# Optimization experiments

Hardware: AMD Instinct MI355X
Metric: run time of the kernel (lower is better)

Reference implementation:

```python
import jax, jax.numpy as jnp
import numpy as np

NUM_HEADS = 16
HEAD_DIM = 64
Q_DIM = K_DIM = V_DIM = 1024
LQ = LK = 4096
TAU = HEAD_DIM ** (-0.5)


def setup_inputs() -> dict:
    key = jax.random.key(0)
    ks = jax.random.split(key, 11)
    inner = NUM_HEADS * HEAD_DIM
    s = 0.02
    return {
        "q": jax.random.normal(ks[0], (LQ, Q_DIM), dtype=jnp.float32),
        "k": jax.random.normal(ks[1], (LK, K_DIM), dtype=jnp.float32),
        "v": jax.random.normal(ks[2], (LK, V_DIM), dtype=jnp.float32),
        "Wq": jax.random.normal(ks[3], (Q_DIM, inner), dtype=jnp.float32) * s,
        "bq": jax.random.normal(ks[4], (inner,), dtype=jnp.float32) * s,
        "Wk": jax.random.normal(ks[5], (K_DIM, inner), dtype=jnp.float32) * s,
        "bk": jax.random.normal(ks[6], (inner,), dtype=jnp.float32) * s,
        "Wv": jax.random.normal(ks[7], (V_DIM, inner), dtype=jnp.float32) * s,
        "bv": jax.random.normal(ks[8], (inner,), dtype=jnp.float32) * s,
        "Wo": jax.random.normal(ks[9], (inner, Q_DIM), dtype=jnp.float32) * s,
        "bo": jax.random.normal(ks[10], (Q_DIM,), dtype=jnp.float32) * s,
    }


def reference(q, k, v, Wq, bq, Wk, bk, Wv, bv, Wo, bo):
    h, x = NUM_HEADS, HEAD_DIM
    # projections: [L, h*x] -> per-head layout
    qh = (q @ Wq + bq).reshape(-1, h, x)  # [Lq, h, x]
    kh = (k @ Wk + bk).reshape(-1, h, x)  # [Lk, h, x]
    vh = (v @ Wv + bv).reshape(-1, h, x)  # [Lk, h, x]
    # scores: [h, Lq, Lk]
    att = jnp.einsum('qhx,khx->hqk', qh, kh) * TAU
    att = jax.nn.softmax(att, axis=-1)  # dropout=0.0 -> identity
    ctx = jnp.einsum('hqk,khx->qhx', att, vh).reshape(-1, h * x)  # [Lq, h*x]
    out = ctx @ Wo + bo  # [Lq, Q_DIM]
    return out, att
```

## Files before the change

### kernel.cpp

```cpp
#include <hip/hip_runtime.h>
#include <hip/hip_bf16.h>

typedef unsigned short ushort_t;
typedef __attribute__((ext_vector_type(8))) short short8;
typedef __attribute__((ext_vector_type(8))) __bf16 bf16x8;
typedef __attribute__((ext_vector_type(4))) float f32x4;

#define LQS 4096
#define LKS 4096
#define NH 16
#define HD 64
#define DIN 1024
#define QBLK 64
#define KVB 64
static constexpr float TAU_S = 0.125f;
static constexpr float LOG2E = 1.4426950408889634f;

__device__ __forceinline__ float exp2_fast(float x) { return __builtin_amdgcn_exp2f(x); }

__device__ __forceinline__ ushort_t f32_to_bf16(float x) {
  union { float f; unsigned u; } v; v.f = x;
  unsigned r = v.u + 0x7FFF + ((v.u >> 16) & 1);
  return (ushort_t)(r >> 16);
}

__device__ __forceinline__ void gld_lds16(const void* g, void* l) {
  __builtin_amdgcn_global_load_lds((const __attribute__((address_space(1))) void*)g,
                                   (__attribute__((address_space(3))) void*)l, 16, 0, 0);
}

__device__ __forceinline__ f32x4 mfma16(bf16x8 a, bf16x8 b, f32x4 c) {
  return __builtin_amdgcn_mfma_f32_16x16x32_bf16(a, b, c, 0, 0, 0);
}

struct Cvt3 { const float* src[3]; ushort_t* dst[3]; };
__global__ void cvt_kernel(Cvt3 c) {
  const float* __restrict__ src = c.src[blockIdx.y];
  ushort_t* __restrict__ dst = c.dst[blockIdx.y];
  int i = (blockIdx.x * 256 + threadIdx.x) * 8;
  float4 a = *(const float4*)(src + i);
  float4 b = *(const float4*)(src + i + 4);
  short8 o;
  o[0] = (short)f32_to_bf16(a.x); o[1] = (short)f32_to_bf16(a.y);
  o[2] = (short)f32_to_bf16(a.z); o[3] = (short)f32_to_bf16(a.w);
  o[4] = (short)f32_to_bf16(b.x); o[5] = (short)f32_to_bf16(b.y);
  o[6] = (short)f32_to_bf16(b.z); o[7] = (short)f32_to_bf16(b.w);
  *(short8*)(dst + i) = o;
}

struct TW4 { const float* W[4]; ushort_t* Wt[4]; };
__global__ void transpose_w(TW4 w) {
  const float* __restrict__ W = w.W[blockIdx.z];
  ushort_t* __restrict__ Wt = w.Wt[blockIdx.z];
  __shared__ float tile[64][65];
  const int t = threadIdx.x;
  const int k0 = blockIdx.y * 64, n0 = blockIdx.x * 64;
#pragma unroll
  for (int i = 0; i < 16; ++i) {
    int idx = i * 256 + t;
    int r = idx >> 6, c = idx & 63;
    tile[r][c] = W[(size_t)(k0 + r) * DIN + n0 + c];
  }
  __syncthreads();
#pragma unroll
  for (int i = 0; i < 16; ++i) {
    int idx = i * 256 + t;
    int r = idx >> 6, c = idx & 63;
    Wt[(size_t)(n0 + r) * DIN + k0 + c] = f32_to_bf16(tile[c][r]);
  }
}

__global__ void transpose_v(const ushort_t* __restrict__ vh, ushort_t* __restrict__ vt) {
  __shared__ ushort_t tile[64][65];
  const int t = threadIdx.x;
  const int k0 = blockIdx.x * 64, h = blockIdx.y;
#pragma unroll
  for (int i = 0; i < 16; ++i) {
    int idx = i * 256 + t;
    int r = idx >> 6, c = idx & 63;
    tile[r][c] = vh[(size_t)(k0 + r) * DIN + h * HD + c];
  }
  __syncthreads();
#pragma unroll
  for (int i = 0; i < 16; ++i) {
    int idx = i * 256 + t;
    int r = idx >> 6, c = idx & 63;
    vt[((size_t)h * HD + r) * (size_t)LKS + k0 + c] = tile[c][r];
  }
}

struct Batch3 {
  const ushort_t* A[3];
  const ushort_t* Bt[3];
  const float* bias[3];
  void* C[3];
  float scale[3];
};
template <bool OUT_F32>
__launch_bounds__(256, 2)
__global__ void gemm_nt(Batch3 bt3) {
  const int bid = blockIdx.x;
  const int xcd = bid & 7, idx = bid >> 3;
  const int z = idx >> 5, rem = idx & 31;
  const int by = xcd * 4 + (rem >> 3), bx = rem & 7;
  const ushort_t* __restrict__ A = bt3.A[z];
  const ushort_t* __restrict__ Bt = bt3.Bt[z];
  const float* __restrict__ bias = bt3.bias[z];
  void* __restrict__ Cout = bt3.C[z];
  const float scale = bt3.scale[z];
  const int K = DIN, N = DIN;

  __shared__ __align__(16) ushort_t Alds[128 * 64];
  __shared__ __align__(16) ushort_t Blds[128 * 64];
  const int t = threadIdx.x, wave = t >> 6, lane = t & 63;
  const int l15 = lane & 15, lg = lane >> 4;
  const int m0 = by * 128, n0 = bx * 128;
  const int wr = wave >> 1, wc = wave & 1;
  f32x4 acc[4][4];
#pragma unroll
  for (int i = 0; i < 4; ++i)
#pragma unroll
    for (int j = 0; j < 4; ++j) acc[i][j] = (f32x4){0.f, 0.f, 0.f, 0.f};

  for (int tk = 0; tk < K / 64; ++tk) {
#pragma unroll
    for (int c = 0; c < 4; ++c) {
      int chunk = wave * 4 + c;
      int row = chunk * 8 + (lane >> 3);
      int ss = (lane & 7) ^ (row & 7);
      gld_lds16(A + (size_t)(m0 + row) * K + tk * 64 + ss * 8, (char*)Alds + chunk * 1024);
      gld_lds16(Bt + (size_t)(n0 + row) * K + tk * 64 + ss * 8, (char*)Blds + chunk * 1024);
    }
    __syncthreads();
#pragma unroll
    for (int kk = 0; kk < 2; ++kk) {
      bf16x8 a[4], b[4];
#pragma unroll
      for (int i = 0; i < 4; ++i) {
        int ra = wr * 64 + i * 16 + l15;
        a[i] = *(const bf16x8*)((const char*)Alds + ra * 128 + ((((kk * 4 + lg) << 4)) ^ ((ra & 7) << 4)));
        int rb = wc * 64 + i * 16 + l15;
        b[i] = *(const bf16x8*)((const char*)Blds + rb * 128 + ((((kk * 4 + lg) << 4)) ^ ((rb & 7) << 4)));
      }
#pragma unroll
      for (int mi = 0; mi < 4; ++mi)
#pragma unroll
        for (int ni = 0; ni < 4; ++ni)
          acc[mi][ni] = mfma16(a[mi], b[ni], acc[mi][ni]);
    }
    __syncthreads();
  }
#pragma unroll
  for (int ni = 0; ni < 4; ++ni) {
    int coln = n0 + wc * 64 + ni * 16 + l15;
    float bv = bias[coln];
#pragma unroll
    for (int mi = 0; mi < 4; ++mi) {
#pragma unroll
      for (int r = 0; r < 4; ++r) {
        int rowm = m0 + wr * 64 + mi * 16 + lg * 4 + r;
        float v = (acc[mi][ni][r] + bv) * scale;
        if (OUT_F32)
          ((float*)Cout)[(size_t)rowm * N + coln] = v;
        else
          ((ushort_t*)Cout)[(size_t)rowm * N + coln] = f32_to_bf16(v);
      }
    }
  }
}

__launch_bounds__(256, 4)
__global__ void attn_kernel(const ushort_t* __restrict__ qh, const ushort_t* __restrict__ kh,
                            const ushort_t* __restrict__ vt, float* __restrict__ att,
                            ushort_t* __restrict__ ctx) {
  __shared__ __align__(16) ushort_t Klds[KVB * 64];
  __shared__ __align__(16) ushort_t Vlds[KVB * 64];
  __shared__ __align__(16) float Patt[4][16 * 64];
  const int t = threadIdx.x, wave = t >> 6, lane = t & 63;
  const int l15 = lane & 15, lg = lane >> 4;
  const int bid = blockIdx.x;
  const int xcd = bid & 7, idx = bid >> 3;
  const int h = xcd * 2 + (idx >> 6);
  const int q0 = (idx & 63) * QBLK;

  char* Pw = (char*)Patt[wave];

  bf16x8 qa[2];
  {
    int row = q0 + wave * 16 + l15;
    const ushort_t* qp = qh + (size_t)row * DIN + h * HD + lg * 8;
    qa[0] = *(const bf16x8*)(qp);
    qa[1] = *(const bf16x8*)(qp + 32);
  }

  const int srow8 = lane >> 3;
  const int sslot = (lane & 7);

  float rs[4] = {0.f, 0.f, 0.f, 0.f};
  for (int tk = 0; tk < LKS / KVB; ++tk) {
#pragma unroll
    for (int c = 0; c < 2; ++c) {
      int chunk = wave * 2 + c;
      int row = chunk * 8 + srow8;
      int ss = sslot ^ (row & 7);
      gld_lds16(kh + (size_t)(tk * KVB + row) * DIN + h * HD + ss * 8, (char*)Klds + chunk * 1024);
    }
    __syncthreads();
#pragma unroll
    for (int ct = 0; ct < 4; ++ct) {
      f32x4 acc = (f32x4){0.f, 0.f, 0.f, 0.f};
#pragma unroll
      for (int kk = 0; kk < 2; ++kk) {
        int row = ct * 16 + l15;
        bf16x8 kb = *(const bf16x8*)((const char*)Klds + row * 128 + ((((kk * 4 + lg) << 4)) ^ ((row & 7) << 4)));
        acc = mfma16(qa[kk], kb, acc);
      }
#pragma unroll
      for (int r = 0; r < 4; ++r) rs[r] += exp2_fast(acc[r]);
    }
    __syncthreads();
  }
#pragma unroll
  for (int m = 1; m < 16; m <<= 1) {
#pragma unroll
    for (int r = 0; r < 4; ++r) rs[r] += __shfl_xor(rs[r], m, 64);
  }
  float recip[4];
#pragma unroll
  for (int r = 0; r < 4; ++r) recip[r] = 1.0f / rs[r];

  f32x4 cacc[4];
#pragma unroll
  for (int x = 0; x < 4; ++x) cacc[x] = (f32x4){0.f, 0.f, 0.f, 0.f};
  float* atth = att + ((size_t)h << 24);

  for (int tk = 0; tk < LKS / KVB; ++tk) {
#pragma unroll
    for (int c = 0; c < 2; ++c) {
      int chunk = wave * 2 + c;
      int row = chunk * 8 + srow8;
      int ss = sslot ^ (row & 7);
      gld_lds16(kh + (size_t)(tk * KVB + row) * DIN + h * HD + ss * 8, (char*)Klds + chunk * 1024);
      gld_lds16(vt + ((size_t)h * HD + row) * (size_t)LKS + tk * KVB + ss * 8, (char*)Vlds + chunk * 1024);
    }
    __syncthreads();
#pragma unroll
    for (int ct = 0; ct < 4; ++ct) {
      f32x4 acc = (f32x4){0.f, 0.f, 0.f, 0.f};
#pragma unroll
      for (int kk = 0; kk < 2; ++kk) {
        int row = ct * 16 + l15;
        bf16x8 kb = *(const bf16x8*)((const char*)Klds + row * 128 + ((((kk * 4 + lg) << 4)) ^ ((row & 7) << 4)));
        acc = mfma16(qa[kk], kb, acc);
      }
#pragma unroll
      for (int r = 0; r < 4; ++r) {
        float p = exp2_fast(acc[r]) * recip[r];
        int R = lg * 4 + r;
        int col = ct * 16 + l15;
        int slot = col >> 2;
        *(float*)(Pw + R * 256 + (((slot ^ R)) << 4) + (col & 3) * 4) = p;
      }
    }
#pragma unroll
    for (int i = 0; i < 4; ++i) {
      int slot = lg + 4 * i;
      f32x4 v = *(const f32x4*)(Pw + l15 * 256 + ((slot ^ l15) << 4));
      int rowq = q0 + wave * 16 + l15;
      *(f32x4*)(atth + (((size_t)rowq) << 12) + tk * KVB + slot * 4) = v;
    }
    bf16x8 pa[2];
#pragma unroll
    for (int kk = 0; kk < 2; ++kk) {
      int s0 = kk * 8 + lg * 2;
      f32x4 lo = *(const f32x4*)(Pw + l15 * 256 + ((s0 ^ l15) << 4));
      f32x4 hi = *(const f32x4*)(Pw + l15 * 256 + (((s0 + 1) ^ l15) << 4));
      short8 sp;
#pragma unroll
      for (int j = 0; j < 4; ++j) {
        sp[j] = (short)f32_to_bf16(lo[j]);
        sp[4 + j] = (short)f32_to_bf16(hi[j]);
      }
      pa[kk] = *(bf16x8*)&sp;
    }
#pragma unroll
    for (int x = 0; x < 4; ++x) {
#pragma unroll
      for (int kk = 0; kk < 2; ++kk) {
        int rv = x * 16 + l15;
        bf16x8 vb = *(const bf16x8*)((const char*)Vlds + rv * 128 + ((((kk * 4 + lg) << 4)) ^ ((rv & 7) << 4)));
        cacc[x] = mfma16(pa[kk], vb, cacc[x]);
      }
    }
    __syncthreads();
  }
#pragma unroll
  for (int x = 0; x < 4; ++x) {
#pragma unroll
    for (int r = 0; r < 4; ++r) {
      int rowq = q0 + wave * 16 + lg * 4 + r;
      int col = h * HD + x * 16 + l15;
      ctx[(size_t)rowq * DIN + col] = f32_to_bf16(cacc[x][r]);
    }
  }
}

extern "C" void kernel_launch(void* const* d_in, const int* in_sizes, int n_in,
                              void* d_out, int out_size, void* d_ws, size_t ws_size,
                              hipStream_t stream) {
  const float* q = (const float*)d_in[0];
  const float* k = (const float*)d_in[1];
  const float* v = (const float*)d_in[2];
  const float* Wq = (const float*)d_in[3];
  const float* bq = (const float*)d_in[4];
  const float* Wk = (const float*)d_in[5];
  const float* bk = (const float*)d_in[6];
  const float* Wv = (const float*)d_in[7];
  const float* bv = (const float*)d_in[8];
  const float* Wo = (const float*)d_in[9];
  const float* bo = (const float*)d_in[10];

  float* out = (float*)d_out;
  float* att = out + (size_t)LQS * DIN;

  char* ws = (char*)d_ws;
  ushort_t* qhb = (ushort_t*)(ws + (size_t)0);
  ushort_t* khb = (ushort_t*)(ws + ((size_t)8 << 20));
  ushort_t* vhb = (ushort_t*)(ws + ((size_t)16 << 20));
  ushort_t* vtb = (ushort_t*)(ws + ((size_t)24 << 20));
  ushort_t* ctx = (ushort_t*)(ws + ((size_t)32 << 20));
  ushort_t* qb = (ushort_t*)(ws + ((size_t)40 << 20));
  ushort_t* kb = (ushort_t*)(ws + ((size_t)48 << 20));
  ushort_t* vb = (ushort_t*)(ws + ((size_t)56 << 20));
  ushort_t* Wqt = (ushort_t*)(ws + ((size_t)64 << 20));
  ushort_t* Wkt = (ushort_t*)(ws + ((size_t)66 << 20));
  ushort_t* Wvt = (ushort_t*)(ws + ((size_t)68 << 20));
  ushort_t* Wot = (ushort_t*)(ws + ((size_t)70 << 20));

  Cvt3 c3;
  c3.src[0] = q; c3.src[1] = k; c3.src[2] = v;
  c3.dst[0] = qb; c3.dst[1] = kb; c3.dst[2] = vb;
  cvt_kernel<<<dim3(LQS * DIN / 8 / 256, 3), 256, 0, stream>>>(c3);

  TW4 w4;
  w4.W[0] = Wq; w4.W[1] = Wk; w4.W[2] = Wv; w4.W[3] = Wo;
  w4.Wt[0] = Wqt; w4.Wt[1] = Wkt; w4.Wt[2] = Wvt; w4.Wt[3] = Wot;
  transpose_w<<<dim3(16, 16, 4), 256, 0, stream>>>(w4);

  Batch3 pb;
  pb.A[0] = qb; pb.A[1] = kb; pb.A[2] = vb;
  pb.Bt[0] = Wqt; pb.Bt[1] = Wkt; pb.Bt[2] = Wvt;
  pb.bias[0] = bq; pb.bias[1] = bk; pb.bias[2] = bv;
  pb.C[0] = qhb; pb.C[1] = khb; pb.C[2] = vhb;
  pb.scale[0] = TAU_S * LOG2E; pb.scale[1] = 1.0f; pb.scale[2] = 1.0f;
  gemm_nt<false><<<768, 256, 0, stream>>>(pb);

  transpose_v<<<dim3(64, 16), 256, 0, stream>>>(vhb, vtb);

  attn_kernel<<<1024, 256, 0, stream>>>(qhb, khb, vtb, att, ctx);

  Batch3 ob;
  ob.A[0] = ctx; ob.A[1] = ctx; ob.A[2] = ctx;
  ob.Bt[0] = Wot; ob.Bt[1] = Wot; ob.Bt[2] = Wot;
  ob.bias[0] = bo; ob.bias[1] = bo; ob.bias[2] = bo;
  ob.C[0] = out; ob.C[1] = out; ob.C[2] = out;
  ob.scale[0] = 1.0f; ob.scale[1] = 1.0f; ob.scale[2] = 1.0f;
  gemm_nt<true><<<256, 256, 0, stream>>>(ob);
}
```

Baseline: 451.9 us.

## Double-buffer GEMM LDS and restructure attention to 32 rows per wave

The projection GEMM gets double-buffered LDS, so the next K tile is prefetched while the current one is computed. The attention kernel drops shared K/V staging and block syncs. Each wave now handles 32 query rows, loading K and V fragments straight from global memory, so each fragment feeds two row groups. Normalisation becomes a log-sum subtracted inside exp2 instead of a reciprocal multiply. The grid is halved and occupancy lowered, and the direct global loads lose LDS sharing across waves, which raises global and L2 traffic in exchange for removing the barriers.

```diff
diff --git a/kernel.cpp b/kernel.cpp
--- a/kernel.cpp
+++ b/kernel.cpp
@@ -11,12 +11,11 @@
 #define NH 16
 #define HD 64
 #define DIN 1024
-#define QBLK 64
-#define KVB 64
 static constexpr float TAU_S = 0.125f;
 static constexpr float LOG2E = 1.4426950408889634f;
 
 __device__ __forceinline__ float exp2_fast(float x) { return __builtin_amdgcn_exp2f(x); }
+__device__ __forceinline__ float log2_fast(float x) { return __builtin_amdgcn_logf(x); }
 
 __device__ __forceinline__ ushort_t f32_to_bf16(float x) {
   union { float f; unsigned u; } v; v.f = x;
@@ -109,38 +108,49 @@
   void* __restrict__ Cout = bt3.C[z];
   const float scale = bt3.scale[z];
   const int K = DIN, N = DIN;
-
-  __shared__ __align__(16) ushort_t Alds[128 * 64];
-  __shared__ __align__(16) ushort_t Blds[128 * 64];
+  const int NT = K / 64;
+
+  __shared__ __align__(16) ushort_t Alds[2][128 * 64];
+  __shared__ __align__(16) ushort_t Blds[2][128 * 64];
   const int t = threadIdx.x, wave = t >> 6, lane = t & 63;
   const int l15 = lane & 15, lg = lane >> 4;
   const int m0 = by * 128, n0 = bx * 128;
   const int wr = wave >> 1, wc = wave & 1;
+
+  const int srow = (wave * 4) * 8 + (lane >> 3);
   f32x4 acc[4][4];
 #pragma unroll
   for (int i = 0; i < 4; ++i)
 #pragma unroll
     for (int j = 0; j < 4; ++j) acc[i][j] = (f32x4){0.f, 0.f, 0.f, 0.f};
 
-  for (int tk = 0; tk < K / 64; ++tk) {
-#pragma unroll
-    for (int c = 0; c < 4; ++c) {
-      int chunk = wave * 4 + c;
-      int row = chunk * 8 + (lane >> 3);
-      int ss = (lane & 7) ^ (row & 7);
-      gld_lds16(A + (size_t)(m0 + row) * K + tk * 64 + ss * 8, (char*)Alds + chunk * 1024);
-      gld_lds16(Bt + (size_t)(n0 + row) * K + tk * 64 + ss * 8, (char*)Blds + chunk * 1024);
-    }
-    __syncthreads();
+#define STAGE(tk, buf)                                                              \
+  {                                                                                 \
+    _Pragma("unroll") for (int c = 0; c < 4; ++c) {                                 \
+      int chunk = wave * 4 + c;                                                     \
+      int row = chunk * 8 + (lane >> 3);                                            \
+      int ss = (lane & 7) ^ (row & 7);                                              \
+      gld_lds16(A + (size_t)(m0 + row) * K + (tk) * 64 + ss * 8,                    \
+                (char*)Alds[buf] + chunk * 1024);                                   \
+      gld_lds16(Bt + (size_t)(n0 + row) * K + (tk) * 64 + ss * 8,                   \
+                (char*)Blds[buf] + chunk * 1024);                                   \
+    }                                                                               \
+  }
+
+  STAGE(0, 0);
+  __syncthreads();
+  int cur = 0;
+  for (int tk = 0; tk < NT; ++tk) {
+    if (tk + 1 < NT) STAGE(tk + 1, cur ^ 1);
 #pragma unroll
     for (int kk = 0; kk < 2; ++kk) {
       bf16x8 a[4], b[4];
 #pragma unroll
       for (int i = 0; i < 4; ++i) {
         int ra = wr * 64 + i * 16 + l15;
-        a[i] = *(const bf16x8*)((const char*)Alds + ra * 128 + ((((kk * 4 + lg) << 4)) ^ ((ra & 7) << 4)));
+        a[i] = *(const bf16x8*)((const char*)Alds[cur] + ra * 128 + ((((kk * 4 + lg) << 4)) ^ ((ra & 7) << 4)));
         int rb = wc * 64 + i * 16 + l15;
-        b[i] = *(const bf16x8*)((const char*)Blds + rb * 128 + ((((kk * 4 + lg) << 4)) ^ ((rb & 7) << 4)));
+        b[i] = *(const bf16x8*)((const char*)Blds[cur] + rb * 128 + ((((kk * 4 + lg) << 4)) ^ ((rb & 7) << 4)));
       }
 #pragma unroll
       for (int mi = 0; mi < 4; ++mi)
@@ -149,7 +159,9 @@
           acc[mi][ni] = mfma16(a[mi], b[ni], acc[mi][ni]);
     }
     __syncthreads();
-  }
+    cur ^= 1;
+  }
+#undef STAGE
 #pragma unroll
   for (int ni = 0; ni < 4; ++ni) {
     int coln = n0 + wc * 64 + ni * 16 + l15;
@@ -169,140 +181,150 @@
   }
 }
 
-__launch_bounds__(256, 4)
+__launch_bounds__(256, 2)
 __global__ void attn_kernel(const ushort_t* __restrict__ qh, const ushort_t* __restrict__ kh,
                             const ushort_t* __restrict__ vt, float* __restrict__ att,
                             ushort_t* __restrict__ ctx) {
-  __shared__ __align__(16) ushort_t Klds[KVB * 64];
-  __shared__ __align__(16) ushort_t Vlds[KVB * 64];
-  __shared__ __align__(16) float Patt[4][16 * 64];
+  __shared__ __align__(16) float Patt[4][2][16 * 64];
   const int t = threadIdx.x, wave = t >> 6, lane = t & 63;
   const int l15 = lane & 15, lg = lane >> 4;
   const int bid = blockIdx.x;
   const int xcd = bid & 7, idx = bid >> 3;
-  const int h = xcd * 2 + (idx >> 6);
-  const int q0 = (idx & 63) * QBLK;
-
-  char* Pw = (char*)Patt[wave];
-
-  bf16x8 qa[2];
-  {
-    int row = q0 + wave * 16 + l15;
-    const ushort_t* qp = qh + (size_t)row * DIN + h * HD + lg * 8;
-    qa[0] = *(const bf16x8*)(qp);
-    qa[1] = *(const bf16x8*)(qp + 32);
-  }
-
-  const int srow8 = lane >> 3;
-  const int sslot = (lane & 7);
-
-  float rs[4] = {0.f, 0.f, 0.f, 0.f};
-  for (int tk = 0; tk < LKS / KVB; ++tk) {
-#pragma unroll
-    for (int c = 0; c < 2; ++c) {
-      int chunk = wave * 2 + c;
-      int row = chunk * 8 + srow8;
-      int ss = sslot ^ (row & 7);
-      gld_lds16(kh + (size_t)(tk * KVB + row) * DIN + h * HD + ss * 8, (char*)Klds + chunk * 1024);
-    }
-    __syncthreads();
+  const int h = xcd * 2 + (idx >> 5);
+  const int q0 = (idx & 31) * 128;
+  const int w0 = q0 + wave * 32;
+
+  bf16x8 qa[2][2];
+#pragma unroll
+  for (int s = 0; s < 2; ++s) {
+    const ushort_t* qp = qh + (size_t)(w0 + s * 16 + l15) * DIN + h * HD + lg * 8;
+    qa[s][0] = *(const bf16x8*)(qp);
+    qa[s][1] = *(const bf16x8*)(qp + 32);
+  }
+
+  const ushort_t* kh_h = kh + h * HD;
+  const ushort_t* vt_h = vt + (size_t)h * HD * LKS;
+
+  float rs[2][4] = {{0.f, 0.f, 0.f, 0.f}, {0.f, 0.f, 0.f, 0.f}};
+  for (int tk = 0; tk < LKS / 64; ++tk) {
+    const ushort_t* kt = kh_h + (size_t)tk * 64 * DIN;
 #pragma unroll
     for (int ct = 0; ct < 4; ++ct) {
-      f32x4 acc = (f32x4){0.f, 0.f, 0.f, 0.f};
-#pragma unroll
-      for (int kk = 0; kk < 2; ++kk) {
-        int row = ct * 16 + l15;
-        bf16x8 kb = *(const bf16x8*)((const char*)Klds + row * 128 + ((((kk * 4 + lg) << 4)) ^ ((row & 7) << 4)));
-        acc = mfma16(qa[kk], kb, acc);
-      }
-#pragma unroll
-      for (int r = 0; r < 4; ++r) rs[r] += exp2_fast(acc[r]);
-    }
-    __syncthreads();
+      const ushort_t* kr = kt + (size_t)(ct * 16 + l15) * DIN + lg * 8;
+      bf16x8 kb0 = *(const bf16x8*)(kr);
+      bf16x8 kb1 = *(const bf16x8*)(kr + 32);
+      f32x4 a0 = (f32x4){0.f, 0.f, 0.f, 0.f};
+      f32x4 a1 = (f32x4){0.f, 0.f, 0.f, 0.f};
+      a0 = mfma16(qa[0][0], kb0, a0);
+      a1 = mfma16(qa[1][0], kb0, a1);
+      a0 = mfma16(qa[0][1], kb1, a0);
+      a1 = mfma16(qa[1][1], kb1, a1);
+#pragma unroll
+      for (int r = 0; r < 4; ++r) {
+        rs[0][r] += exp2_fast(a0[r]);
+        rs[1][r] += exp2_fast(a1[r]);
+      }
+    }
   }
 #pragma unroll
   for (int m = 1; m < 16; m <<= 1) {
 #pragma unroll
-    for (int r = 0; r < 4; ++r) rs[r] += __shfl_xor(rs[r], m, 64);
-  }
-  float recip[4];
-#pragma unroll
-  for (int r = 0; r < 4; ++r) recip[r] = 1.0f / rs[r];
-
-  f32x4 cacc[4];
-#pragma unroll
-  for (int x = 0; x < 4; ++x) cacc[x] = (f32x4){0.f, 0.f, 0.f, 0.f};
+    for (int s = 0; s < 2; ++s)
+#pragma unroll
+      for (int r = 0; r < 4; ++r) rs[s][r] += __shfl_xor(rs[s][r], m, 64);
+  }
+  float lrs[2][4];
+#pragma unroll
+  for (int s = 0; s < 2; ++s)
+#pragma unroll
+    for (int r = 0; r < 4; ++r) lrs[s][r] = log2_fast(rs[s][r]);
+
+  f32x4 cacc[2][4];
+#pragma unroll
+  for (int s = 0; s < 2; ++s)
+#pragma unroll
+    for (int x = 0; x < 4; ++x) cacc[s][x] = (f32x4){0.f, 0.f, 0.f, 0.f};
   float* atth = att + ((size_t)h << 24);
-
-  for (int tk = 0; tk < LKS / KVB; ++tk) {
-#pragma unroll
-    for (int c = 0; c < 2; ++c) {
-      int chunk = wave * 2 + c;
-      int row = chunk * 8 + srow8;
-      int ss = sslot ^ (row & 7);
-      gld_lds16(kh + (size_t)(tk * KVB + row) * DIN + h * HD + ss * 8, (char*)Klds + chunk * 1024);
-      gld_lds16(vt + ((size_t)h * HD + row) * (size_t)LKS + tk * KVB + ss * 8, (char*)Vlds + chunk * 1024);
-    }
-    __syncthreads();
+  char* Pw0 = (char*)Patt[wave][0];
+  char* Pw1 = (char*)Patt[wave][1];
+
+  for (int tk = 0; tk < LKS / 64; ++tk) {
+    const ushort_t* kt = kh_h + (size_t)tk * 64 * DIN;
+    const ushort_t* vtt = vt_h + tk * 64;
+    bf16x8 vb[4][2];
+#pragma unroll
+    for (int x = 0; x < 4; ++x) {
+      const ushort_t* vr = vtt + (size_t)(x * 16 + l15) * LKS + lg * 8;
+      vb[x][0] = *(const bf16x8*)(vr);
+      vb[x][1] = *(const bf16x8*)(vr + 32);
+    }
 #pragma unroll
     for (int ct = 0; ct < 4; ++ct) {
-      f32x4 acc = (f32x4){0.f, 0.f, 0.f, 0.f};
-#pragma unroll
-      for (int kk = 0; kk < 2; ++kk) {
-        int row = ct * 16 + l15;
-        bf16x8 kb = *(const bf16x8*)((const char*)Klds + row * 128 + ((((kk * 4 + lg) << 4)) ^ ((row & 7) << 4)));
-        acc = mfma16(qa[kk], kb, acc);
-      }
+      const ushort_t* kr = kt + (size_t)(ct * 16 + l15) * DIN + lg * 8;
+      bf16x8 kb0 = *(const bf16x8*)(kr);
+      bf16x8 kb1 = *(const bf16x8*)(kr + 32);
+      f32x4 a0 = (f32x4){0.f, 0.f, 0.f, 0.f};
+      f32x4 a1 = (f32x4){0.f, 0.f, 0.f, 0.f};
+      a0 = mfma16(qa[0][0], kb0, a0);
+      a1 = mfma16(qa[1][0], kb0, a1);
+      a0 = mfma16(qa[0][1], kb1, a0);
+      a1 = mfma16(qa[1][1], kb1, a1);
+      int col = ct * 16 + l15;
+      int slot = col >> 2;
+      int coff = (col & 3) * 4;
 #pragma unroll
       for (int r = 0; r < 4; ++r) {
-        float p = exp2_fast(acc[r]) * recip[r];
         int R = lg * 4 + r;
-        int col = ct * 16 + l15;
-        int slot = col >> 2;
-        *(float*)(Pw + R * 256 + (((slot ^ R)) << 4) + (col & 3) * 4) = p;
+        float p0 = exp2_fast(a0[r] - lrs[0][r]);
+        float p1 = exp2_fast(a1[r] - lrs[1][r]);
+        *(float*)(Pw0 + R * 256 + ((slot ^ R) << 4) + coff) = p0;
+        *(float*)(Pw1 + R * 256 + ((slot ^ R) << 4) + coff) = p1;
       }
     }
 #pragma unroll
     for (int i = 0; i < 4; ++i) {
       int slot = lg + 4 * i;
-      f32x4 v = *(const f32x4*)(Pw + l15 * 256 + ((slot ^ l15) << 4));
-      int rowq = q0 + wave * 16 + l15;
-      *(f32x4*)(atth + (((size_t)rowq) << 12) + tk * KVB + slot * 4) = v;
-    }
-    bf16x8 pa[2];
-#pragma unroll
-    for (int kk = 0; kk < 2; ++kk) {
-      int s0 = kk * 8 + lg * 2;
-      f32x4 lo = *(const f32x4*)(Pw + l15 * 256 + ((s0 ^ l15) << 4));
-      f32x4 hi = *(const f32x4*)(Pw + l15 * 256 + (((s0 + 1) ^ l15) << 4));
-      short8 sp;
-#pragma unroll
-      for (int j = 0; j < 4; ++j) {
-        sp[j] = (short)f32_to_bf16(lo[j]);
-        sp[4 + j] = (short)f32_to_bf16(hi[j]);
-      }
-      pa[kk] = *(bf16x8*)&sp;
-    }
+      f32x4 v0 = *(const f32x4*)(Pw0 + l15 * 256 + ((slot ^ l15) << 4));
+      f32x4 v1 = *(const f32x4*)(Pw1 + l15 * 256 + ((slot ^ l15) << 4));
+      size_t base = ((size_t)(w0 + l15) << 12) + tk * 64 + slot * 4;
+      *(f32x4*)(atth + base) = v0;
+      *(f32x4*)(atth + base + (16 << 12)) = v1;
+    }
+#pragma unroll
+    for (int s = 0; s < 2; ++s) {
+      char* Pw = s ? Pw1 : Pw0;
+      bf16x8 pa[2];
+#pragma unroll
+      for (int kk = 0; kk < 2; ++kk) {
+        int s0 = kk * 8 + lg * 2;
+        f32x4 lo = *(const f32x4*)(Pw + l15 * 256 + ((s0 ^ l15) << 4));
+        f32x4 hi = *(const f32x4*)(Pw + l15 * 256 + (((s0 + 1) ^ l15) << 4));
+        short8 sp;
+#pragma unroll
+        for (int j = 0; j < 4; ++j) {
+          sp[j] = (short)f32_to_bf16(lo[j]);
+          sp[4 + j] = (short)f32_to_bf16(hi[j]);
+        }
+        pa[kk] = *(bf16x8*)&sp;
+      }
+#pragma unroll
+      for (int x = 0; x < 4; ++x) {
+        cacc[s][x] = mfma16(pa[0], vb[x][0], cacc[s][x]);
+        cacc[s][x] = mfma16(pa[1], vb[x][1], cacc[s][x]);
+      }
+    }
+  }
+#pragma unroll
+  for (int s = 0; s < 2; ++s)
 #pragma unroll
     for (int x = 0; x < 4; ++x) {
 #pragma unroll
-      for (int kk = 0; kk < 2; ++kk) {
-        int rv = x * 16 + l15;
-        bf16x8 vb = *(const bf16x8*)((const char*)Vlds + rv * 128 + ((((kk * 4 + lg) << 4)) ^ ((rv & 7) << 4)));
-        cacc[x] = mfma16(pa[kk], vb, cacc[x]);
-      }
-    }
-    __syncthreads();
-  }
-#pragma unroll
-  for (int x = 0; x < 4; ++x) {
-#pragma unroll
-    for (int r = 0; r < 4; ++r) {
-      int rowq = q0 + wave * 16 + lg * 4 + r;
-      int col = h * HD + x * 16 + l15;
-      ctx[(size_t)rowq * DIN + col] = f32_to_bf16(cacc[x][r]);
-    }
-  }
+      for (int r = 0; r < 4; ++r) {
+        int rowq = w0 + s * 16 + lg * 4 + r;
+        int col = h * HD + x * 16 + l15;
+        ctx[(size_t)rowq * DIN + col] = f32_to_bf16(cacc[s][x][r]);
+      }
+    }
 }
 
 extern "C" void kernel_launch(void* const* d_in, const int* in_sizes, int n_in,
@@ -357,7 +379,7 @@
 
   transpose_v<<<dim3(64, 16), 256, 0, stream>>>(vhb, vtb);
 
-  attn_kernel<<<1024, 256, 0, stream>>>(qhb, khb, vtb, att, ctx);
+  attn_kernel<<<512, 256, 0, stream>>>(qhb, khb, vtb, att, ctx);
 
   Batch3 ob;
   ob.A[0] = ctx; ob.A[1] = ctx; ob.A[2] = ctx;
```

Measured after the change: 632.5 us. +40.0%, slower.
